# Kernel tuning notes

Measured on AMD Instinct MI355X. Metric: run time of the kernel, lower is better.

## Reference

```python
import jax, jax.numpy as jnp
import numpy as np

B, CIN, H, W = 4, 128, 64, 64
PL, ATT, R = 256, 64, 16   # planes, planes//4, MD_R
STEPS = 6                   # TRAIN_STEPS default
EPS = 1e-6


def _l2norm(v, axis):
    return v / jnp.maximum(jnp.linalg.norm(v, axis=axis, keepdims=True), 1e-12)


def setup_inputs() -> dict:
    key = jax.random.key(0)
    ks = jax.random.split(key, 11)
    s = 0.05
    return {
        "x": jax.random.normal(ks[0], (B, CIN, H, W), jnp.float32),
        "conv1_w": jax.random.normal(ks[1], (PL, CIN), jnp.float32) * s,      # 1x1 conv, no bias
        "conv3_w": jax.random.normal(ks[2], (PL, 1, 3, 3), jnp.float32) * s,  # depthwise 3x3
        "conv3_b": jax.random.normal(ks[3], (PL,), jnp.float32) * s,
        "lower_w": jax.random.normal(ks[4], (PL, PL), jnp.float32) * s,       # Conv1d k=1
        "lower_b": jax.random.normal(ks[5], (PL,), jnp.float32) * s,
        "ca1_w": jax.random.normal(ks[6], (ATT, PL), jnp.float32) * s,        # channel attn 1x1
        "ca2_w": jax.random.normal(ks[7], (PL, ATT), jnp.float32) * s,
        "fc_w": jax.random.normal(ks[8], (CIN, PL), jnp.float32) * s,         # fc_adapt_channels1
        "fc_b": jax.random.normal(ks[9], (CIN,), jnp.float32) * s,
        "bases_init": jax.random.uniform(ks[10], (B * H * W, 1, R), jnp.float32),  # rand_init bases
    }


def reference(x, conv1_w, conv3_w, conv3_b, lower_w, lower_b, ca1_w, ca2_w, fc_w, fc_b, bases_init):
    # conv1 (1x1, no bias) then depthwise 3x3 (groups=PL)
    y = jnp.einsum('bchw,oc->bohw', x, conv1_w)
    y = jax.lax.conv_general_dilated(y, conv3_w, (1, 1), 'SAME',
                                     dimension_numbers=('NCHW', 'OIHW', 'NCHW'),
                                     feature_group_count=PL)
    y = y + conv3_b[None, :, None, None]
    # '(b s) c h w -> (b h w) c s' with s=1 -> tokens [M, C]
    xm = jnp.transpose(y, (0, 2, 3, 1)).reshape(B * H * W, PL)
    # Hamburger lower_bread: Conv1d(k=1) + ReLU
    xl = jax.nn.relu(xm @ lower_w.T + lower_b)
    xn = xl[:, None, :]                        # NMF x: [M, D=1, N=C]
    # NMF2D local_inference (torch.no_grad in original)
    xs = jax.lax.stop_gradient(xn)
    bases = _l2norm(bases_init, 1)             # [M, 1, R]
    coef = jax.nn.softmax(jnp.einsum('mdn,mdr->mnr', xs, bases), axis=-1)  # inv_t=1
    for _ in range(STEPS):
        num = jnp.einsum('mdn,mdr->mnr', xs, bases)
        den = jnp.einsum('mnr,mrk->mnk', coef, jnp.einsum('mdr,mdk->mrk', bases, bases))
        coef = coef * num / (den + EPS)
        num = jnp.einsum('mdn,mnr->mdr', xs, coef)
        den = jnp.einsum('mdr,mrk->mdk', bases, jnp.einsum('mnr,mnk->mrk', coef, coef))
        bases = bases * num / (den + EPS)
    bases = jax.lax.stop_gradient(bases)
    coef = jax.lax.stop_gradient(coef)
    # compute_coef (differentiable via xn)
    num = jnp.einsum('mdn,mdr->mnr', xn, bases)
    den = jnp.einsum('mnr,mrk->mnk', coef, jnp.einsum('mdr,mdk->mrk', bases, bases))
    coef = coef * num / (den + EPS)
    xr = jnp.einsum('mdr,mnr->mn', bases, coef)     # bases @ coef^T, [M, C] (D=1 squeezed)
    feat = jax.nn.relu(xm + xr)                     # Hamburger residual + ReLU
    # mean over s (s=1) and back to [B, C, H, W]
    feat = jnp.transpose(feat.reshape(B, H, W, PL), (0, 3, 1, 2))
    # AMPooling channel attention
    avg = feat.mean(axis=(2, 3))
    mx = feat.max(axis=(2, 3))
    ca = lambda v: jax.nn.relu(v @ ca1_w.T) @ ca2_w.T
    att = jax.nn.sigmoid(ca(avg) + ca(mx))          # [B, C]
    out = feat * att[:, :, None, None]
    out = jnp.einsum('bchw,oc->bohw', out, fc_w) + fc_b[None, :, None, None]
    return out, att[:, :, None, None]
```

## Files before the change

### kernel.cpp

```cpp
#include <hip/hip_runtime.h>
#include <hip/hip_bf16.h>
#include <math.h>

#define EPS 1e-6f
#define PITCH 72

typedef short s16x8 __attribute__((ext_vector_type(8)));
typedef float f32x4 __attribute__((ext_vector_type(4)));

__device__ __forceinline__ short bf16of(float f) {
  __hip_bfloat16 h = __float2bfloat16(f);
  return __builtin_bit_cast(short, h);
}

__global__ __launch_bounds__(256) void k_conv1x1(const float* __restrict__ x,
                                                 const float* __restrict__ w1,
                                                 float* __restrict__ y) {
  __shared__ __align__(16) short Aw[256 * PITCH];
  __shared__ __align__(16) short Xs[64 * PITCH];
  const int t = threadIdx.x;
  const int m0 = blockIdx.x * 64;
  const int img = m0 >> 12, hw0 = m0 & 4095;
  const int lane = t & 63, w = t >> 6;
  const int lrow = lane & 15, lk = (lane >> 4) * 8;
  f32x4 acc[8][2];
#pragma unroll
  for (int i = 0; i < 8; ++i)
#pragma unroll
    for (int j = 0; j < 2; ++j) acc[i][j] = {0.f, 0.f, 0.f, 0.f};

  for (int kk = 0; kk < 128; kk += 64) {
    __syncthreads();
    {
      const float* wp = w1 + (size_t)t * 128 + kk;
#pragma unroll
      for (int q = 0; q < 16; ++q) {
        const float4 v = *(const float4*)(wp + q * 4);
        short4 sv = {bf16of(v.x), bf16of(v.y), bf16of(v.z), bf16of(v.w)};
        *(short4*)(&Aw[t * PITCH + q * 4]) = sv;
      }
    }
    {
      const int m4 = (t & 15) * 4;
      const int cg = (t >> 4) * 4;
      float4 col[4];
#pragma unroll
      for (int cc = 0; cc < 4; ++cc)
        col[cc] = *(const float4*)(x + (size_t)(img * 128 + kk + cg + cc) * 4096 + hw0 + m4);
#pragma unroll
      for (int r = 0; r < 4; ++r) {
        short4 sv = {bf16of(((const float*)&col[0])[r]),
                     bf16of(((const float*)&col[1])[r]),
                     bf16of(((const float*)&col[2])[r]),
                     bf16of(((const float*)&col[3])[r])};
        *(short4*)(&Xs[(m4 + r) * PITCH + cg]) = sv;
      }
    }
    __syncthreads();
#pragma unroll
    for (int ks = 0; ks < 2; ++ks) {
      const int ko = ks * 32 + lk;
      s16x8 bfr[2];
#pragma unroll
      for (int j = 0; j < 2; ++j)
        bfr[j] = *(const s16x8*)(&Xs[(((w >> 1) * 2 + j) * 16 + lrow) * PITCH + ko]);
#pragma unroll
      for (int i = 0; i < 8; ++i) {
        const s16x8 af = *(const s16x8*)(&Aw[(((w & 1) * 8 + i) * 16 + lrow) * PITCH + ko]);
#pragma unroll
        for (int j = 0; j < 2; ++j)
          acc[i][j] = __builtin_amdgcn_mfma_f32_16x16x32_bf16(af, bfr[j], acc[i][j], 0, 0, 0);
      }
    }
  }
#pragma unroll
  for (int i = 0; i < 8; ++i) {
    const int p = ((w & 1) * 8 + i) * 16 + (lane >> 4) * 4;
#pragma unroll
    for (int j = 0; j < 2; ++j) {
      const int m = m0 + ((w >> 1) * 2 + j) * 16 + lrow;
      *(f32x4*)(y + (size_t)m * 256 + p) = acc[i][j];
    }
  }
}

__global__ __launch_bounds__(256) void k_dwconv(const float* __restrict__ y,
                                                const float* __restrict__ w3,
                                                const float* __restrict__ b3,
                                                float* __restrict__ xm) {
  __shared__ float wt[9][256];
  __shared__ float bs[256];
  const int t = threadIdx.x;
#pragma unroll
  for (int i = 0; i < 9; ++i) wt[i][t] = w3[t * 9 + i];
  bs[t] = b3[t];
  __syncthreads();
  const int sub = t >> 6;
  const int pq = t & 63;
  const int m = blockIdx.x * 4 + sub;
  const int hw = m & 4095;
  const int h = hw >> 6, ww = hw & 63;
  const int bb = m >> 12;
  float4 acc = *(const float4*)(&bs[pq * 4]);
#pragma unroll
  for (int dy = -1; dy <= 1; ++dy) {
    const int hh = h + dy;
    if (hh < 0 || hh > 63) continue;
#pragma unroll
    for (int dx = -1; dx <= 1; ++dx) {
      const int w2 = ww + dx;
      if (w2 < 0 || w2 > 63) continue;
      const int idx = (dy + 1) * 3 + (dx + 1);
      const float4 v =
          *(const float4*)(y + (size_t)((bb << 12) + (hh << 6) + w2) * 256 + pq * 4);
      const float4 wv = *(const float4*)(&wt[idx][pq * 4]);
      acc.x += v.x * wv.x;
      acc.y += v.y * wv.y;
      acc.z += v.z * wv.z;
      acc.w += v.w * wv.w;
    }
  }
  *(float4*)(xm + (size_t)m * 256 + pq * 4) = acc;
}

__global__ __launch_bounds__(256) void k_lower(const float* __restrict__ xm,
                                               const float* __restrict__ lw,
                                               const float* __restrict__ lb,
                                               float* __restrict__ xl) {
  __shared__ __align__(16) short Aw[256 * PITCH];
  __shared__ __align__(16) short Xs[64 * PITCH];
  const int t = threadIdx.x;
  const int m0 = blockIdx.x * 64;
  const int lane = t & 63, w = t >> 6;
  const int lrow = lane & 15, lk = (lane >> 4) * 8;
  f32x4 acc[8][2];
#pragma unroll
  for (int i = 0; i < 8; ++i)
#pragma unroll
    for (int j = 0; j < 2; ++j) acc[i][j] = {0.f, 0.f, 0.f, 0.f};

  for (int kk = 0; kk < 256; kk += 64) {
    __syncthreads();
    {
      const float* wp = lw + (size_t)t * 256 + kk;
#pragma unroll
      for (int q = 0; q < 16; ++q) {
        const float4 v = *(const float4*)(wp + q * 4);
        short4 sv = {bf16of(v.x), bf16of(v.y), bf16of(v.z), bf16of(v.w)};
        *(short4*)(&Aw[t * PITCH + q * 4]) = sv;
      }
    }
    {
      const int m = t & 63, q = t >> 6;
      const float* xp = xm + (size_t)(m0 + m) * 256 + kk + q * 16;
#pragma unroll
      for (int jj = 0; jj < 4; ++jj) {
        const float4 v = *(const float4*)(xp + jj * 4);
        short4 sv = {bf16of(v.x), bf16of(v.y), bf16of(v.z), bf16of(v.w)};
        *(short4*)(&Xs[m * PITCH + q * 16 + jj * 4]) = sv;
      }
    }
    __syncthreads();
#pragma unroll
    for (int ks = 0; ks < 2; ++ks) {
      const int ko = ks * 32 + lk;
      s16x8 bfr[2];
#pragma unroll
      for (int j = 0; j < 2; ++j)
        bfr[j] = *(const s16x8*)(&Xs[(((w >> 1) * 2 + j) * 16 + lrow) * PITCH + ko]);
#pragma unroll
      for (int i = 0; i < 8; ++i) {
        const s16x8 af = *(const s16x8*)(&Aw[(((w & 1) * 8 + i) * 16 + lrow) * PITCH + ko]);
#pragma unroll
        for (int j = 0; j < 2; ++j)
          acc[i][j] = __builtin_amdgcn_mfma_f32_16x16x32_bf16(af, bfr[j], acc[i][j], 0, 0, 0);
      }
    }
  }
#pragma unroll
  for (int i = 0; i < 8; ++i) {
    const int n = ((w & 1) * 8 + i) * 16 + (lane >> 4) * 4;
    const float4 bias = *(const float4*)(lb + n);
#pragma unroll
    for (int j = 0; j < 2; ++j) {
      const int m = m0 + ((w >> 1) * 2 + j) * 16 + lrow;
      f32x4 v = acc[i][j];
      v.x = fmaxf(v.x + bias.x, 0.f);
      v.y = fmaxf(v.y + bias.y, 0.f);
      v.z = fmaxf(v.z + bias.z, 0.f);
      v.w = fmaxf(v.w + bias.w, 0.f);
      *(f32x4*)(xl + (size_t)m * 256 + n) = v;
    }
  }
}

__global__ __launch_bounds__(256) void k_em_fast(const float* xl,
                                                 const float* __restrict__ binit,
                                                 const float* __restrict__ xmp,
                                                 float* feat) {
  const int lane = threadIdx.x & 63;
  const int m = blockIdx.x * 4 + (threadIdx.x >> 6);
  const float bv0 = binit[m * 16 + (lane & 15)];
  const float bn0 = bv0 / fmaxf(fabsf(bv0), 1e-12f);
  if (!__all(bn0 == 1.0f)) return;
  const float4 s4 = *(const float4*)(xl + (size_t)m * 256 + lane * 4);
  const float s[4] = {s4.x, s4.y, s4.z, s4.w};
  float C[4] = {0.0625f, 0.0625f, 0.0625f, 0.0625f};
  float Bv = 1.f;
  for (int step = 0; step < 6; ++step) {
    const float k1 = 16.f * Bv * Bv;
    float pnum = 0.f, psq = 0.f;
#pragma unroll
    for (int i = 0; i < 4; ++i) {
      const float den = fmaf(C[i], k1, EPS);
      const float cn = C[i] * (s[i] * Bv) * __builtin_amdgcn_rcpf(den);
      C[i] = cn;
      pnum = fmaf(s[i], cn, pnum);
      psq = fmaf(cn, cn, psq);
    }
#pragma unroll
    for (int d = 1; d < 64; d <<= 1) {
      pnum += __shfl_xor(pnum, d, 64);
      psq += __shfl_xor(psq, d, 64);
    }
    const float den2 = fmaf(16.f * Bv, psq, EPS);
    Bv = Bv * pnum * __builtin_amdgcn_rcpf(den2);
  }
  const float4 xm4 = *(const float4*)(xmp + (size_t)m * 256 + lane * 4);
  const float xmv[4] = {xm4.x, xm4.y, xm4.z, xm4.w};
  const float k1 = 16.f * Bv * Bv;
  float o[4];
#pragma unroll
  for (int i = 0; i < 4; ++i) {
    const float den = fmaf(C[i], k1, EPS);
    const float cn = C[i] * (s[i] * Bv) * __builtin_amdgcn_rcpf(den);
    const float xr = 16.f * Bv * cn;
    o[i] = fmaxf(xmv[i] + xr, 0.f);
  }
  const float4 outv = {o[0], o[1], o[2], o[3]};
  *(float4*)(feat + (size_t)m * 256 + lane * 4) = outv;
}

__global__ __launch_bounds__(256, 2) void k_em_slow(const float* xl,
                                                    const float* __restrict__ binit,
                                                    const float* __restrict__ xmp,
                                                    float* feat) {
  const int lane = threadIdx.x & 63;
  const int m = blockIdx.x * 4 + (threadIdx.x >> 6);
  const float bv0 = binit[m * 16 + (lane & 15)];
  const float bn0 = bv0 / fmaxf(fabsf(bv0), 1e-12f);
  if (__all(bn0 == 1.0f)) return;
  const float4 s4 = *(const float4*)(xl + (size_t)m * 256 + lane * 4);
  const float s[4] = {s4.x, s4.y, s4.z, s4.w};
  float b[16];
#pragma unroll
  for (int r = 0; r < 16; ++r) {
    const float v = binit[m * 16 + r];
    b[r] = v / fmaxf(fabsf(v), 1e-12f);
  }
  float c[4][16];
#pragma unroll
  for (int i = 0; i < 4; ++i) {
    float mx = s[i] * b[0];
#pragma unroll
    for (int r = 1; r < 16; ++r) mx = fmaxf(mx, s[i] * b[r]);
    float sum = 0.f;
#pragma unroll
    for (int r = 0; r < 16; ++r) {
      const float e = __expf(s[i] * b[r] - mx);
      c[i][r] = e;
      sum += e;
    }
    const float inv = __fdividef(1.f, sum);
#pragma unroll
    for (int r = 0; r < 16; ++r) c[i][r] *= inv;
  }
  for (int step = 0; step < 6; ++step) {
    float red[32];
#pragma unroll
    for (int r = 0; r < 32; ++r) red[r] = 0.f;
#pragma unroll
    for (int i = 0; i < 4; ++i) {
      float tt = 0.f;
#pragma unroll
      for (int r = 0; r < 16; ++r) tt += c[i][r] * b[r];
      float tp = 0.f;
#pragma unroll
      for (int r = 0; r < 16; ++r) {
        const float cn = c[i][r] * (s[i] * b[r]) * __frcp_rn(tt * b[r] + EPS);
        c[i][r] = cn;
        tp += cn * b[r];
        red[r] += s[i] * cn;
      }
#pragma unroll
      for (int r = 0; r < 16; ++r) red[16 + r] += tp * c[i][r];
    }
    int cnt = 32;
#pragma unroll
    for (int k = 4; k >= 0; --k) {
      const int d = 1 << k;
      const bool up = (lane >> k) & 1;
      const int half = cnt >> 1;
#pragma unroll
      for (int j = 0; j < half; ++j) {
        const float lo = red[j], hi = red[j + half];
        const float send = up ? lo : hi;
        const float recv = __shfl_xor(send, d, 64);
        red[j] = (up ? hi : lo) + recv;
      }
      cnt = half;
    }
    float S = red[0] + __shfl_xor(red[0], 32, 64);
    const float dpart = __shfl_xor(S, 16, 64);
    const float q = S * __frcp_rn(dpart + EPS);
#pragma unroll
    for (int r = 0; r < 16; ++r) b[r] *= __shfl(q, r, 64);
  }
  const float4 xm4 = *(const float4*)(xmp + (size_t)m * 256 + lane * 4);
  const float xmv[4] = {xm4.x, xm4.y, xm4.z, xm4.w};
  float o4[4];
#pragma unroll
  for (int i = 0; i < 4; ++i) {
    float tt = 0.f;
#pragma unroll
    for (int r = 0; r < 16; ++r) tt += c[i][r] * b[r];
    float xr = 0.f;
#pragma unroll
    for (int r = 0; r < 16; ++r) {
      const float cn = c[i][r] * (s[i] * b[r]) * __frcp_rn(tt * b[r] + EPS);
      xr += b[r] * cn;
    }
    o4[i] = fmaxf(xmv[i] + xr, 0.f);
  }
  const float4 outv = {o4[0], o4[1], o4[2], o4[3]};
  *(float4*)(feat + (size_t)m * 256 + lane * 4) = outv;
}

__global__ __launch_bounds__(256) void k_pool1(const float* __restrict__ feat,
                                               float* __restrict__ psum,
                                               float* __restrict__ pmax) {
  const int t = threadIdx.x;
  const int b = blockIdx.x >> 6;
  const int ch = blockIdx.x & 63;
  const float* fp = feat + (size_t)(b * 4096 + ch * 64) * 256 + t;
  float sum = 0.f, mx = -1e30f;
#pragma unroll 8
  for (int r = 0; r < 64; ++r) {
    const float v = fp[(size_t)r * 256];
    sum += v;
    mx = fmaxf(mx, v);
  }
  psum[(size_t)blockIdx.x * 256 + t] = sum;
  pmax[(size_t)blockIdx.x * 256 + t] = mx;
}

__global__ __launch_bounds__(256) void k_att(const float* __restrict__ psum,
                                             const float* __restrict__ pmax,
                                             const float* __restrict__ ca1,
                                             const float* __restrict__ ca2,
                                             float* __restrict__ attv,
                                             float* __restrict__ out_att) {
  __shared__ float sA[256], sM[256], sH[64];
  const int t = threadIdx.x;
  const int b = blockIdx.x;
  float sum = 0.f, mx = -1e30f;
#pragma unroll 8
  for (int ch = 0; ch < 64; ++ch) {
    sum += psum[(size_t)(b * 64 + ch) * 256 + t];
    mx = fmaxf(mx, pmax[(size_t)(b * 64 + ch) * 256 + t]);
  }
  sA[t] = sum * (1.0f / 4096.0f);
  sM[t] = mx;
  __syncthreads();
  if (t < 64) {
    float ha = 0.f, hm = 0.f;
#pragma unroll 8
    for (int p = 0; p < 256; ++p) {
      const float w = ca1[t * 256 + p];
      ha += sA[p] * w;
      hm += sM[p] * w;
    }
    sH[t] = fmaxf(ha, 0.f) + fmaxf(hm, 0.f);
  }
  __syncthreads();
  float logit = 0.f;
#pragma unroll 8
  for (int a = 0; a < 64; ++a) logit += sH[a] * ca2[t * 64 + a];
  const float av = 1.0f / (1.0f + expf(-logit));
  attv[b * 256 + t] = av;
  out_att[b * 256 + t] = av;
}

__global__ __launch_bounds__(256) void k_fc(const float* __restrict__ feat,
                                            const float* __restrict__ attv,
                                            const float* __restrict__ fw,
                                            const float* __restrict__ fb,
                                            float* __restrict__ out) {
  __shared__ __align__(16) short Fs[64 * PITCH];
  __shared__ __align__(16) short Ws[128 * PITCH];
  const int t = threadIdx.x;
  const int m0 = blockIdx.x * 64;
  const int img = m0 >> 12, hw0 = m0 & 4095;
  const int lane = t & 63, w = t >> 6;
  const int lrow = lane & 15, lk = (lane >> 4) * 8;
  f32x4 acc[2][4];
#pragma unroll
  for (int i = 0; i < 2; ++i)
#pragma unroll
    for (int j = 0; j < 4; ++j) acc[i][j] = {0.f, 0.f, 0.f, 0.f};

  for (int kk = 0; kk < 256; kk += 64) {
    __syncthreads();
    {
      const int m = t & 63, q = t >> 6;
      const float* fp = feat + (size_t)(m0 + m) * 256 + kk + q * 16;
      const float* ap = attv + img * 256 + kk + q * 16;
#pragma unroll
      for (int jj = 0; jj < 4; ++jj) {
        const float4 v = *(const float4*)(fp + jj * 4);
        const float4 a = *(const float4*)(ap + jj * 4);
        short4 sv = {bf16of(v.x * a.x), bf16of(v.y * a.y), bf16of(v.z * a.z),
                     bf16of(v.w * a.w)};
        *(short4*)(&Fs[m * PITCH + q * 16 + jj * 4]) = sv;
      }
    }
    {
      const int o = t & 127, q = t >> 7;
      const float* wp = fw + (size_t)o * 256 + kk + q * 32;
#pragma unroll
      for (int jj = 0; jj < 8; ++jj) {
        const float4 v = *(const float4*)(wp + jj * 4);
        short4 sv = {bf16of(v.x), bf16of(v.y), bf16of(v.z), bf16of(v.w)};
        *(short4*)(&Ws[o * PITCH + q * 32 + jj * 4]) = sv;
      }
    }
    __syncthreads();
#pragma unroll
    for (int ks = 0; ks < 2; ++ks) {
      const int ko = ks * 32 + lk;
      s16x8 af[2];
#pragma unroll
      for (int i = 0; i < 2; ++i)
        af[i] = *(const s16x8*)(&Fs[(((w & 1) * 2 + i) * 16 + lrow) * PITCH + ko]);
#pragma unroll
      for (int j = 0; j < 4; ++j) {
        const s16x8 bfr = *(const s16x8*)(&Ws[(((w >> 1) * 4 + j) * 16 + lrow) * PITCH + ko]);
#pragma unroll
        for (int i = 0; i < 2; ++i)
          acc[i][j] = __builtin_amdgcn_mfma_f32_16x16x32_bf16(af[i], bfr, acc[i][j], 0, 0, 0);
      }
    }
  }
#pragma unroll
  for (int j = 0; j < 4; ++j) {
    const int o = ((w >> 1) * 4 + j) * 16 + lrow;
    const float bias = fb[o];
#pragma unroll
    for (int i = 0; i < 2; ++i) {
      const int hw = hw0 + ((w & 1) * 2 + i) * 16 + (lane >> 4) * 4;
      f32x4 v = acc[i][j];
      v.x += bias;
      v.y += bias;
      v.z += bias;
      v.w += bias;
      *(f32x4*)(out + (size_t)img * 524288 + (size_t)o * 4096 + hw) = v;
    }
  }
}

extern "C" void kernel_launch(void* const* d_in, const int* in_sizes, int n_in,
                              void* d_out, int out_size, void* d_ws, size_t ws_size,
                              hipStream_t stream) {
  const float* x = (const float*)d_in[0];
  const float* w1 = (const float*)d_in[1];
  const float* w3 = (const float*)d_in[2];
  const float* b3 = (const float*)d_in[3];
  const float* lw = (const float*)d_in[4];
  const float* lb = (const float*)d_in[5];
  const float* ca1 = (const float*)d_in[6];
  const float* ca2 = (const float*)d_in[7];
  const float* fw = (const float*)d_in[8];
  const float* fb = (const float*)d_in[9];
  const float* binit = (const float*)d_in[10];

  float* ws = (float*)d_ws;
  float* bufA = ws;
  float* bufB = ws + 4194304;
  float* psum = ws + 8388608;
  float* pmax = psum + 65536;
  float* attv = pmax + 65536;
  float* out = (float*)d_out;
  float* out_att = out + 2097152;

  const dim3 blk(256);
  k_conv1x1<<<dim3(256), blk, 0, stream>>>(x, w1, bufA);
  k_dwconv<<<dim3(4096), blk, 0, stream>>>(bufA, w3, b3, bufB);
  k_lower<<<dim3(256), blk, 0, stream>>>(bufB, lw, lb, bufA);
  k_em_fast<<<dim3(4096), blk, 0, stream>>>(bufA, binit, bufB, bufA);
  k_em_slow<<<dim3(4096), blk, 0, stream>>>(bufA, binit, bufB, bufA);
  k_pool1<<<dim3(256), blk, 0, stream>>>(bufA, psum, pmax);
  k_att<<<dim3(4), blk, 0, stream>>>(psum, pmax, ca1, ca2, attv, out_att);
  k_fc<<<dim3(256), blk, 0, stream>>>(bufA, attv, fw, fb, out);
}
```

Measured before the change: 94.55 us.

## Fuse lower GEMM, fast EM and pooling partials into one kernel

The lower-bread GEMM output is kept in LDS and the fast rank-constant NMF path runs directly on it inside the same kernel. The fused kernel also accumulates per-block channel sum and max partials, so the global round trip for xl and the separate pooling read of feat are removed. Rows that need the general path are written to a fallback buffer and flagged, and the slow EM and pool-fix kernels only run for flagged blocks. The cost is that EM work is serialized over 16 rows per wave with far fewer waves in flight, and the kernel uses more LDS.

```diff
diff --git a/kernel.cpp b/kernel.cpp
--- a/kernel.cpp
+++ b/kernel.cpp
@@ -123,12 +123,18 @@
   *(float4*)(xm + (size_t)m * 256 + pq * 4) = acc;
 }
 
-__global__ __launch_bounds__(256) void k_lower(const float* __restrict__ xm,
-                                               const float* __restrict__ lw,
-                                               const float* __restrict__ lb,
-                                               float* __restrict__ xl) {
-  __shared__ __align__(16) short Aw[256 * PITCH];
-  __shared__ __align__(16) short Xs[64 * PITCH];
+__global__ __launch_bounds__(256, 2) void k_lower_em(
+    const float* __restrict__ xm, const float* __restrict__ lw,
+    const float* __restrict__ lb, const float* __restrict__ binit,
+    float* feat, float* __restrict__ xl_fb, float* __restrict__ psum,
+    float* __restrict__ pmax, int* __restrict__ flag) {
+  __shared__ __align__(16) char smem[74768];
+  short* Aw = (short*)smem;
+  short* Xs = (short*)(smem + 36864);
+  float* xlL = (float*)smem;
+  float* psL = (float*)(smem + 66560);
+  float* pmL = (float*)(smem + 70656);
+  int* sflag = (int*)(smem + 74752);
   const int t = threadIdx.x;
   const int m0 = blockIdx.x * 64;
   const int lane = t & 63, w = t >> 6;
@@ -177,74 +183,95 @@
       }
     }
   }
+  __syncthreads();
+  if (t == 0) *sflag = 0;
 #pragma unroll
   for (int i = 0; i < 8; ++i) {
     const int n = ((w & 1) * 8 + i) * 16 + (lane >> 4) * 4;
     const float4 bias = *(const float4*)(lb + n);
 #pragma unroll
     for (int j = 0; j < 2; ++j) {
-      const int m = m0 + ((w >> 1) * 2 + j) * 16 + lrow;
+      const int mr = ((w >> 1) * 2 + j) * 16 + lrow;
       f32x4 v = acc[i][j];
       v.x = fmaxf(v.x + bias.x, 0.f);
       v.y = fmaxf(v.y + bias.y, 0.f);
       v.z = fmaxf(v.z + bias.z, 0.f);
       v.w = fmaxf(v.w + bias.w, 0.f);
-      *(f32x4*)(xl + (size_t)m * 256 + n) = v;
-    }
-  }
-}
-
-__global__ __launch_bounds__(256) void k_em_fast(const float* xl,
-                                                 const float* __restrict__ binit,
-                                                 const float* __restrict__ xmp,
-                                                 float* feat) {
-  const int lane = threadIdx.x & 63;
-  const int m = blockIdx.x * 4 + (threadIdx.x >> 6);
-  const float bv0 = binit[m * 16 + (lane & 15)];
-  const float bn0 = bv0 / fmaxf(fabsf(bv0), 1e-12f);
-  if (!__all(bn0 == 1.0f)) return;
-  const float4 s4 = *(const float4*)(xl + (size_t)m * 256 + lane * 4);
-  const float s[4] = {s4.x, s4.y, s4.z, s4.w};
-  float C[4] = {0.0625f, 0.0625f, 0.0625f, 0.0625f};
-  float Bv = 1.f;
-  for (int step = 0; step < 6; ++step) {
+      *(f32x4*)(&xlL[mr * 260 + n]) = v;
+    }
+  }
+  __syncthreads();
+
+  float ps4[4] = {0.f, 0.f, 0.f, 0.f};
+  float pm4[4] = {-1e30f, -1e30f, -1e30f, -1e30f};
+  for (int pi = 0; pi < 16; ++pi) {
+    const int mr = w * 16 + pi;
+    const int m = m0 + mr;
+    const float bv0 = binit[m * 16 + (lane & 15)];
+    const float bn0 = bv0 / fmaxf(fabsf(bv0), 1e-12f);
+    const f32x4 s4v = *(const f32x4*)(&xlL[mr * 260 + lane * 4]);
+    if (!__all(bn0 == 1.0f)) {
+      *(f32x4*)(xl_fb + (size_t)m * 256 + lane * 4) = s4v;
+      if (lane == 0) *sflag = 1;
+      continue;
+    }
+    const float s[4] = {s4v.x, s4v.y, s4v.z, s4v.w};
+    float C[4] = {0.0625f, 0.0625f, 0.0625f, 0.0625f};
+    float Bv = 1.f;
+    for (int step = 0; step < 6; ++step) {
+      const float k1 = 16.f * Bv * Bv;
+      float pnum = 0.f, psq = 0.f;
+#pragma unroll
+      for (int i = 0; i < 4; ++i) {
+        const float den = fmaf(C[i], k1, EPS);
+        const float cn = C[i] * (s[i] * Bv) * __builtin_amdgcn_rcpf(den);
+        C[i] = cn;
+        pnum = fmaf(s[i], cn, pnum);
+        psq = fmaf(cn, cn, psq);
+      }
+#pragma unroll
+      for (int d = 1; d < 64; d <<= 1) {
+        pnum += __shfl_xor(pnum, d, 64);
+        psq += __shfl_xor(psq, d, 64);
+      }
+      const float den2 = fmaf(16.f * Bv, psq, EPS);
+      Bv = Bv * pnum * __builtin_amdgcn_rcpf(den2);
+    }
+    const float4 xm4 = *(const float4*)(xm + (size_t)m * 256 + lane * 4);
+    const float xmv[4] = {xm4.x, xm4.y, xm4.z, xm4.w};
     const float k1 = 16.f * Bv * Bv;
-    float pnum = 0.f, psq = 0.f;
+    float o[4];
 #pragma unroll
     for (int i = 0; i < 4; ++i) {
       const float den = fmaf(C[i], k1, EPS);
       const float cn = C[i] * (s[i] * Bv) * __builtin_amdgcn_rcpf(den);
-      C[i] = cn;
-      pnum = fmaf(s[i], cn, pnum);
-      psq = fmaf(cn, cn, psq);
-    }
-#pragma unroll
-    for (int d = 1; d < 64; d <<= 1) {
-      pnum += __shfl_xor(pnum, d, 64);
-      psq += __shfl_xor(psq, d, 64);
-    }
-    const float den2 = fmaf(16.f * Bv, psq, EPS);
-    Bv = Bv * pnum * __builtin_amdgcn_rcpf(den2);
-  }
-  const float4 xm4 = *(const float4*)(xmp + (size_t)m * 256 + lane * 4);
-  const float xmv[4] = {xm4.x, xm4.y, xm4.z, xm4.w};
-  const float k1 = 16.f * Bv * Bv;
-  float o[4];
+      const float xr = 16.f * Bv * cn;
+      o[i] = fmaxf(xmv[i] + xr, 0.f);
+      ps4[i] += o[i];
+      pm4[i] = fmaxf(pm4[i], o[i]);
+    }
+    const f32x4 outv = {o[0], o[1], o[2], o[3]};
+    *(f32x4*)(feat + (size_t)m * 256 + lane * 4) = outv;
+  }
 #pragma unroll
   for (int i = 0; i < 4; ++i) {
-    const float den = fmaf(C[i], k1, EPS);
-    const float cn = C[i] * (s[i] * Bv) * __builtin_amdgcn_rcpf(den);
-    const float xr = 16.f * Bv * cn;
-    o[i] = fmaxf(xmv[i] + xr, 0.f);
-  }
-  const float4 outv = {o[0], o[1], o[2], o[3]};
-  *(float4*)(feat + (size_t)m * 256 + lane * 4) = outv;
+    psL[w * 256 + lane * 4 + i] = ps4[i];
+    pmL[w * 256 + lane * 4 + i] = pm4[i];
+  }
+  __syncthreads();
+  const float sv = psL[t] + psL[256 + t] + psL[512 + t] + psL[768 + t];
+  const float mv = fmaxf(fmaxf(pmL[t], pmL[256 + t]), fmaxf(pmL[512 + t], pmL[768 + t]));
+  psum[(size_t)blockIdx.x * 256 + t] = sv;
+  pmax[(size_t)blockIdx.x * 256 + t] = mv;
+  if (t == 0) flag[blockIdx.x] = *sflag;
 }
 
 __global__ __launch_bounds__(256, 2) void k_em_slow(const float* xl,
                                                     const float* __restrict__ binit,
                                                     const float* __restrict__ xmp,
-                                                    float* feat) {
+                                                    float* feat,
+                                                    const int* __restrict__ flag) {
+  if (flag[blockIdx.x >> 4] == 0) return;
   const int lane = threadIdx.x & 63;
   const int m = blockIdx.x * 4 + (threadIdx.x >> 6);
   const float bv0 = binit[m * 16 + (lane & 15)];
@@ -336,13 +363,14 @@
   *(float4*)(feat + (size_t)m * 256 + lane * 4) = outv;
 }
 
-__global__ __launch_bounds__(256) void k_pool1(const float* __restrict__ feat,
-                                               float* __restrict__ psum,
-                                               float* __restrict__ pmax) {
+__global__ __launch_bounds__(256) void k_pool_fix(const float* __restrict__ feat,
+                                                  const int* __restrict__ flag,
+                                                  float* __restrict__ psum,
+                                                  float* __restrict__ pmax) {
+  const int bid = blockIdx.x;
+  if (flag[bid] == 0) return;
   const int t = threadIdx.x;
-  const int b = blockIdx.x >> 6;
-  const int ch = blockIdx.x & 63;
-  const float* fp = feat + (size_t)(b * 4096 + ch * 64) * 256 + t;
+  const float* fp = feat + (size_t)bid * 64 * 256 + t;
   float sum = 0.f, mx = -1e30f;
 #pragma unroll 8
   for (int r = 0; r < 64; ++r) {
@@ -350,8 +378,8 @@
     sum += v;
     mx = fmaxf(mx, v);
   }
-  psum[(size_t)blockIdx.x * 256 + t] = sum;
-  pmax[(size_t)blockIdx.x * 256 + t] = mx;
+  psum[(size_t)bid * 256 + t] = sum;
+  pmax[(size_t)bid * 256 + t] = mx;
 }
 
 __global__ __launch_bounds__(256) void k_att(const float* __restrict__ psum,
@@ -486,19 +514,21 @@
   float* ws = (float*)d_ws;
   float* bufA = ws;
   float* bufB = ws + 4194304;
-  float* psum = ws + 8388608;
+  float* bufC = ws + 8388608;
+  float* psum = ws + 12582912;
   float* pmax = psum + 65536;
   float* attv = pmax + 65536;
+  int* flag = (int*)(attv + 1024);
   float* out = (float*)d_out;
   float* out_att = out + 2097152;
 
   const dim3 blk(256);
   k_conv1x1<<<dim3(256), blk, 0, stream>>>(x, w1, bufA);
   k_dwconv<<<dim3(4096), blk, 0, stream>>>(bufA, w3, b3, bufB);
-  k_lower<<<dim3(256), blk, 0, stream>>>(bufB, lw, lb, bufA);
-  k_em_fast<<<dim3(4096), blk, 0, stream>>>(bufA, binit, bufB, bufA);
-  k_em_slow<<<dim3(4096), blk, 0, stream>>>(bufA, binit, bufB, bufA);
-  k_pool1<<<dim3(256), blk, 0, stream>>>(bufA, psum, pmax);
+  k_lower_em<<<dim3(256), blk, 0, stream>>>(bufB, lw, lb, binit, bufA, bufC,
+                                            psum, pmax, flag);
+  k_em_slow<<<dim3(4096), blk, 0, stream>>>(bufC, binit, bufB, bufA, flag);
+  k_pool_fix<<<dim3(256), blk, 0, stream>>>(bufA, flag, psum, pmax);
   k_att<<<dim3(4), blk, 0, stream>>>(psum, pmax, ca1, ca2, attv, out_att);
   k_fc<<<dim3(256), blk, 0, stream>>>(bufA, attv, fw, fb, out);
 }
```

Result: slower. 110.7 us (+17.1%).
